# Kernel tuning notes

Measured on AMD Instinct MI355X. Metric: run time of the kernel, lower is better.

## Reference

```python
import jax, jax.numpy as jnp
import numpy as np

B = 64        # graphs per batch
N0 = 131072   # total nodes (2048 per graph)
E = 1048576   # total edges (within-graph)
H = 128       # hidden_size
C = 7         # class_num (input feature dim)
EPS = 1e-5


def setup_inputs() -> dict:
    key = jax.random.key(0)
    ks = jax.random.split(key, 16)
    n0 = N0 // B
    x = jax.random.normal(ks[0], (N0, C), dtype=jnp.float32)
    # within-graph random edges: edge e belongs to graph e // (E//B)
    g = jnp.repeat(jnp.arange(B, dtype=jnp.int32), E // B)
    row = jax.random.randint(ks[1], (E,), 0, n0, dtype=jnp.int32) + g * n0
    col = jax.random.randint(ks[2], (E,), 0, n0, dtype=jnp.int32) + g * n0
    edge_index = jnp.stack([row, col], axis=0)
    batch = jnp.repeat(jnp.arange(B, dtype=jnp.int32), n0)
    s = 0.05
    params = dict(
        Wc1=jax.random.normal(ks[3], (C, H), jnp.float32) * s,     # conv1 weight
        Wc=jax.random.normal(ks[4], (3, H, H), jnp.float32) * s,   # conv2-4 weights
        bc=jax.random.normal(ks[5], (4, H), jnp.float32) * s,      # conv biases
        Wf=jax.random.normal(ks[6], (4, H, H), jnp.float32) * s,   # fc weights
        bf=jax.random.normal(ks[7], (4, H), jnp.float32) * s,      # fc biases
        bn_g=jnp.ones((4, H), jnp.float32),                        # BN gamma
        bn_b=jnp.zeros((4, H), jnp.float32),                       # BN beta
        Ws1=jax.random.normal(ks[8], (4, H, 1), jnp.float32) * s,  # SAG GraphConv root weight
        Ws2=jax.random.normal(ks[9], (4, H, 1), jnp.float32) * s,  # SAG GraphConv neighbor weight
        bs=jax.random.normal(ks[10], (4, 1), jnp.float32) * s,     # SAG GraphConv bias
    )
    return dict(x=x, edge_index=edge_index, batch=batch, **params)


def _gcn_conv(x, W, b, row, col, m, N):
    # PyG GCNConv with self loops: out_i = sum_{j->i} h_j / sqrt(d_i d_j) + h_i / d_i + b
    h = x @ W
    deg = jax.ops.segment_sum(m, col, num_segments=N) + 1.0  # +1 for self loop
    dis = jax.lax.rsqrt(deg)
    norm = dis[row] * dis[col] * m  # masked-out edges contribute 0
    agg = jax.ops.segment_sum(h[row] * norm[:, None], col, num_segments=N)
    return agg + h * (dis * dis)[:, None] + b


def _sag_score(x, W1, W2, b, row, col, m, N):
    # GraphConv(H, 1, aggr='add'): score_i = W1^T x_i + W2^T sum_{j->i} x_j + b
    nbr = jax.ops.segment_sum(x[row] * m[:, None], col, num_segments=N)
    return (x @ W1 + nbr @ W2 + b).reshape(-1)


def _bn(x, g, b):
    mu = jnp.mean(x, axis=0)
    var = jnp.mean((x - mu) ** 2, axis=0)  # biased, matches torch BN training
    return (x - mu) * jax.lax.rsqrt(var + EPS) * g + b


def reference(x, edge_index, batch, Wc1, Wc, bc, Wf, bf, bn_g, bn_b, Ws1, Ws2, bs):
    row, col = edge_index[0], edge_index[1]
    m = jnp.ones(row.shape, x.dtype)  # edge validity mask (static-size edge list)
    n = x.shape[0] // B               # nodes per graph (equal-size graphs)
    for i in range(4):
        N = B * n
        W = Wc1 if i == 0 else Wc[i - 1]
        h = _gcn_conv(x, W, bc[i], row, col, m, N)
        h = jax.nn.relu(h @ Wf[i] + bf[i])
        h = _bn(h, bn_g[i], bn_b[i])
        # SAGPooling(ratio=0.5): per-graph top-k by GraphConv score, x *= tanh(score)
        score = _sag_score(h, Ws1[i], Ws2[i], bs[i], row, col, m, N)
        k = n // 2
        _, idx = jax.lax.top_k(score.reshape(B, n), k)  # [B, k] per-graph indices
        perm = (idx + jnp.arange(B, dtype=idx.dtype)[:, None] * n).reshape(-1)
        x = h[perm] * jnp.tanh(score[perm])[:, None]
        # re-index edges; mask edges touching removed nodes
        inv = jnp.full((N,), -1, dtype=row.dtype).at[perm].set(
            jnp.arange(B * k, dtype=row.dtype))
        nr, nc = inv[row], inv[col]
        valid = (nr >= 0) & (nc >= 0)
        m = m * valid.astype(m.dtype)
        row = jnp.where(valid, nr, 0)
        col = jnp.where(valid, nc, 0)
        n = k
    # global_mean_pool over block-structured batch -> [B, H]
    return x.reshape(B, n, -1).mean(axis=1)
```

## Files before the change

kernel.cpp:

```cpp
#include <hip/hip_runtime.h>
#include <cstdint>

#define HB 128
#define NB 64
#define NE 1048576
#define EG (NE / 256)

__global__ __launch_bounds__(256) void init_edges_k(const int* __restrict__ ei,
    int* __restrict__ row, int* __restrict__ col, int E) {
  int e = blockIdx.x * blockDim.x + threadIdx.x;
  if (e < E) { row[e] = ei[e]; col[e] = ei[E + e]; }
}

__global__ __launch_bounds__(128) void init_goff_k(int* __restrict__ goff, int epg) {
  int g = threadIdx.x;
  if (g <= NB) goff[g] = g * epg;
}

__global__ __launch_bounds__(256) void matmulK_k(const float* __restrict__ X,
    const float* __restrict__ W, const float* __restrict__ bias,
    float* __restrict__ out, int N, int K, int KS, int flags) {
  extern __shared__ float lw[];
  int tid = threadIdx.x;
  int nv = K * 32;
  for (int idx = tid; idx < nv; idx += 256)
    ((float4*)lw)[idx] = ((const float4*)W)[idx];
  __syncthreads();
  int tx = tid & 31, ty = tid >> 5;
  long rowbase = (long)blockIdx.x * 32;
  float acc[4][4] = {};
  const float* xp = X + (size_t)(rowbase + ty) * KS;
  for (int k = 0; k < K; ++k) {
    float4 wv = ((float4*)lw)[k * 32 + tx];
    #pragma unroll
    for (int rr = 0; rr < 4; ++rr) {
      float xv = xp[(size_t)rr * 8 * KS + k];
      acc[rr][0] += xv * wv.x; acc[rr][1] += xv * wv.y;
      acc[rr][2] += xv * wv.z; acc[rr][3] += xv * wv.w;
    }
  }
  float4 bv = make_float4(0.f, 0.f, 0.f, 0.f);
  if (flags & 1) bv = ((const float4*)bias)[tx];
  #pragma unroll
  for (int rr = 0; rr < 4; ++rr) {
    long r = rowbase + ty + rr * 8;
    float4 v;
    v.x = acc[rr][0] + bv.x; v.y = acc[rr][1] + bv.y;
    v.z = acc[rr][2] + bv.z; v.w = acc[rr][3] + bv.w;
    if (flags & 2) {
      v.x = fmaxf(v.x, 0.f); v.y = fmaxf(v.y, 0.f);
      v.z = fmaxf(v.z, 0.f); v.w = fmaxf(v.w, 0.f);
    }
    ((float4*)(out + (size_t)r * HB))[tx] = v;
  }
}

__global__ __launch_bounds__(256) void gemm128_k(const float* __restrict__ X,
    const float* __restrict__ W, const float* __restrict__ bias,
    float* __restrict__ out, int N, int flags,
    const int* __restrict__ sel, const float* __restrict__ scale,
    const float* __restrict__ bnsc, float* __restrict__ stat) {
  __shared__ float Xs[2][64][8];
  __shared__ float2 red[8][128];
  int tid = threadIdx.x;
  int tx = tid & 31;
  int ty = tid >> 5;
  long rowbase = (long)blockIdx.x * 64;
  float4 acc[8];
  #pragma unroll
  for (int r = 0; r < 8; ++r) acc[r] = make_float4(0.f, 0.f, 0.f, 0.f);
  int lr = tid >> 1, lq = (tid & 1) * 4;
  const float* xrow = nullptr;
  float lsc = 1.f;
  bool gmode = (flags & 4) != 0;
  if (tid < 128) {
    long srcrow = rowbase + lr;
    if (gmode) { srcrow = sel[rowbase + lr]; lsc = scale[rowbase + lr]; }
    xrow = X + (size_t)srcrow * HB + lq;
  }
  auto loadx = [&](int kc) -> float4 {
    float4 v = *(const float4*)(xrow + kc * 8);
    if (gmode) {
      int ch = kc * 8 + lq;
      float4 a = *(const float4*)(bnsc + ch);
      float4 b = *(const float4*)(bnsc + 128 + ch);
      v.x = (v.x * a.x + b.x) * lsc; v.y = (v.y * a.y + b.y) * lsc;
      v.z = (v.z * a.z + b.z) * lsc; v.w = (v.w * a.w + b.w) * lsc;
    } else {
      v.x *= lsc; v.y *= lsc; v.z *= lsc; v.w *= lsc;
    }
    return v;
  };
  if (tid < 128) *(float4*)&Xs[0][lr][lq] = loadx(0);
  __syncthreads();
  for (int kc = 0; kc < 16; ++kc) {
    int cur = kc & 1;
    if (kc < 15 && tid < 128)
      *(float4*)&Xs[cur ^ 1][lr][lq] = loadx(kc + 1);
    float4 wreg[8];
    #pragma unroll
    for (int k = 0; k < 8; ++k)
      wreg[k] = *(const float4*)(W + (size_t)(kc * 8 + k) * HB + 4 * tx);
    #pragma unroll
    for (int kk = 0; kk < 8; kk += 4) {
      float4 xreg[8];
      #pragma unroll
      for (int r = 0; r < 8; ++r)
        xreg[r] = *(const float4*)&Xs[cur][ty + 8 * r][kk];
      #pragma unroll
      for (int k = 0; k < 4; ++k) {
        #pragma unroll
        for (int r = 0; r < 8; ++r) {
          float xv = ((const float*)&xreg[r])[k];
          float4 wv = wreg[kk + k];
          acc[r].x += xv * wv.x; acc[r].y += xv * wv.y;
          acc[r].z += xv * wv.z; acc[r].w += xv * wv.w;
        }
      }
    }
    __syncthreads();
  }
  float4 bv = make_float4(0.f, 0.f, 0.f, 0.f);
  if (flags & 1) bv = ((const float4*)bias)[tx];
  float4 psum = make_float4(0.f, 0.f, 0.f, 0.f);
  float4 psq  = make_float4(0.f, 0.f, 0.f, 0.f);
  #pragma unroll
  for (int r = 0; r < 8; ++r) {
    float4 v;
    v.x = acc[r].x + bv.x; v.y = acc[r].y + bv.y;
    v.z = acc[r].z + bv.z; v.w = acc[r].w + bv.w;
    if (flags & 2) {
      v.x = fmaxf(v.x, 0.f); v.y = fmaxf(v.y, 0.f);
      v.z = fmaxf(v.z, 0.f); v.w = fmaxf(v.w, 0.f);
    }
    if (flags & 8) {
      psum.x += v.x; psum.y += v.y; psum.z += v.z; psum.w += v.w;
      psq.x += v.x * v.x; psq.y += v.y * v.y;
      psq.z += v.z * v.z; psq.w += v.w * v.w;
    }
    *(float4*)(out + (size_t)(rowbase + ty + 8 * r) * HB + 4 * tx) = v;
  }
  if (flags & 8) {
    red[ty][4 * tx + 0] = make_float2(psum.x, psq.x);
    red[ty][4 * tx + 1] = make_float2(psum.y, psq.y);
    red[ty][4 * tx + 2] = make_float2(psum.z, psq.z);
    red[ty][4 * tx + 3] = make_float2(psum.w, psq.w);
    __syncthreads();
    if (tid < 128) {
      float s = 0.f, q = 0.f;
      #pragma unroll
      for (int t = 0; t < 8; ++t) { s += red[t][tid].x; q += red[t][tid].y; }
      atomicAdd(&stat[tid], s);
      atomicAdd(&stat[128 + tid], q);
    }
  }
}

__global__ __launch_bounds__(1024) void csr_build_k(const int* __restrict__ row,
    const int* __restrict__ col, const int* __restrict__ goff,
    float* __restrict__ dis, int* __restrict__ off, int* __restrict__ srow,
    float* __restrict__ snorm, int n) {
  extern __shared__ int lds[];
  int* ldeg = lds;
  int* lsa  = lds + n;
  int* lsb  = lds + 2 * n;
  float* ldis = (float*)(lds + 3 * n);
  int g = blockIdx.x, tid = threadIdx.x;
  int e0 = goff[g], e1 = goff[g + 1];
  int base = g * n;
  for (int i = tid; i < n; i += 1024) ldeg[i] = 0;
  __syncthreads();
  for (int e = e0 + tid; e < e1; e += 1024) atomicAdd(&ldeg[col[e] - base], 1);
  __syncthreads();
  for (int i = tid; i < n; i += 1024) {
    int d = ldeg[i];
    ldis[i] = rsqrtf((float)d + 1.f);
    lsa[i] = d;
  }
  __syncthreads();
  int* src = lsa; int* dst = lsb;
  for (int o = 1; o < n; o <<= 1) {
    for (int i = tid; i < n; i += 1024) dst[i] = src[i] + ((i >= o) ? src[i - o] : 0);
    __syncthreads();
    int* t = src; src = dst; dst = t;
  }
  for (int i = tid; i < n; i += 1024) {
    int d = ldeg[i];
    int ex = src[i] - d;
    off[base + i] = e0 + ex;
    ldeg[i] = ex;
    dis[base + i] = ldis[i];
  }
  if (tid == 0) off[base + n] = e1;
  __syncthreads();
  for (int e = e0 + tid; e < e1; e += 1024) {
    int r = row[e], c = col[e];
    int lc = c - base;
    int p = e0 + atomicAdd(&ldeg[lc], 1);
    srow[p] = r;
    snorm[p] = ldis[r - base] * ldis[lc];
  }
}

__global__ __launch_bounds__(256) void agg7_k(const float* __restrict__ x,
    const int* __restrict__ srow, const float* __restrict__ snorm,
    const int* __restrict__ off, const float* __restrict__ dis,
    float* __restrict__ aggx, int N) {
  int gid = blockIdx.x * blockDim.x + threadIdx.x;
  int node = gid >> 3, c = gid & 7;
  if (node >= N) return;
  float acc = 0.f;
  if (c < 7) {
    int s = off[node], e = off[node + 1];
    for (int j = s; j < e; ++j) acc += x[(size_t)srow[j] * 7 + c] * snorm[j];
    float d = dis[node];
    acc += x[(size_t)node * 7 + c] * d * d;
  }
  aggx[(size_t)node * 8 + c] = acc;
}

__global__ __launch_bounds__(256) void gather_combine_k(const float* __restrict__ hw,
    const int* __restrict__ srow, const float* __restrict__ snorm,
    const int* __restrict__ off, const float* __restrict__ dis,
    const float* __restrict__ bc, float* __restrict__ out, int N) {
  int gid = blockIdx.x * blockDim.x + threadIdx.x;
  int node = gid >> 5;
  if (node >= N) return;
  int ch = (gid & 31) * 4;
  int s = off[node], e = off[node + 1];
  float4 acc = make_float4(0.f, 0.f, 0.f, 0.f);
  for (int j = s; j < e; ++j) {
    int r = srow[j];
    float nm = snorm[j];
    float4 v = *(const float4*)(hw + (size_t)r * HB + ch);
    acc.x += v.x * nm; acc.y += v.y * nm; acc.z += v.z * nm; acc.w += v.w * nm;
  }
  float d = dis[node], d2 = d * d;
  float4 h = *(const float4*)(hw + (size_t)node * HB + ch);
  float4 b = *(const float4*)(bc + ch);
  acc.x += h.x * d2 + b.x; acc.y += h.y * d2 + b.y;
  acc.z += h.z * d2 + b.z; acc.w += h.w * d2 + b.w;
  *(float4*)(out + (size_t)node * HB + ch) = acc;
}

__global__ __launch_bounds__(128) void bnfin_k(float* __restrict__ stat,
    const float* __restrict__ g, const float* __restrict__ b,
    float* __restrict__ sc, int N) {
  int c = threadIdx.x;
  if (c < 128) {
    float mu = stat[c] / N, ms = stat[128 + c] / N;
    float var = ms - mu * mu;
    float a = g[c] * rsqrtf(var + 1e-5f);
    sc[c] = a;
    sc[128 + c] = b[c] - mu * a;
    stat[c] = 0.f;
    stat[128 + c] = 0.f;
  }
}

__global__ __launch_bounds__(256) void score_prep_k(const float* __restrict__ h,
    const float* __restrict__ sc, const float* __restrict__ w1,
    const float* __restrict__ w2, float* __restrict__ selfs,
    float* __restrict__ t2, int N) {
  int gid = blockIdx.x * blockDim.x + threadIdx.x;
  int node = gid >> 6;
  if (node >= N) return;
  int lane = gid & 63, c = lane * 2;
  float2 v = *(const float2*)(h + (size_t)node * HB + c);
  v.x = v.x * sc[c] + sc[128 + c];
  v.y = v.y * sc[c + 1] + sc[128 + c + 1];
  float s1 = v.x * w1[c] + v.y * w1[c + 1];
  float s2 = v.x * w2[c] + v.y * w2[c + 1];
  #pragma unroll
  for (int off = 32; off > 0; off >>= 1) {
    s1 += __shfl_xor(s1, off);
    s2 += __shfl_xor(s2, off);
  }
  if (lane == 0) { selfs[node] = s1; t2[node] = s2; }
}

__global__ __launch_bounds__(256) void score_k(const float* __restrict__ selfs,
    const float* __restrict__ t2, const int* __restrict__ srow,
    const int* __restrict__ off, const float* __restrict__ bs,
    float* __restrict__ score, int N) {
  int i = blockIdx.x * blockDim.x + threadIdx.x;
  if (i >= N) return;
  float s = selfs[i] + bs[0];
  int e0 = off[i], e1 = off[i + 1];
  for (int j = e0; j < e1; ++j) s += t2[srow[j]];
  score[i] = s;
}

__global__ __launch_bounds__(256) void rank_topk_k(const float* __restrict__ score,
    int* __restrict__ inv, int* __restrict__ sel, float* __restrict__ scale,
    int n, int k, int bpg) {
  extern __shared__ float ls[];
  int g = blockIdx.x / bpg, sub = blockIdx.x % bpg;
  int tid = threadIdx.x;
  const float* sg = score + (size_t)g * n;
  for (int i = tid; i < n; i += 256) ls[i] = sg[i];
  __syncthreads();
  int i0 = sub * 256 + tid;
  float s0 = ls[i0];
  int r0 = 0;
  for (int jb = 0; jb < n; jb += 4) {
    float4 v = *(const float4*)(ls + jb);
    r0 += (v.x > s0) || (v.x == s0 && (jb + 0) < i0);
    r0 += (v.y > s0) || (v.y == s0 && (jb + 1) < i0);
    r0 += (v.z > s0) || (v.z == s0 && (jb + 2) < i0);
    r0 += (v.w > s0) || (v.w == s0 && (jb + 3) < i0);
  }
  if (r0 < k) {
    inv[(size_t)g * n + i0] = g * k + r0;
    sel[(size_t)g * k + r0] = g * n + i0;
    scale[(size_t)g * k + r0] = tanhf(s0);
  } else inv[(size_t)g * n + i0] = -1;
}

__global__ __launch_bounds__(256) void gather_x_k(const float* __restrict__ h,
    const float* __restrict__ bnsc, const int* __restrict__ sel,
    const float* __restrict__ scale, float* __restrict__ xout, int M) {
  int gid = blockIdx.x * blockDim.x + threadIdx.x;
  int r = gid >> 5;
  if (r >= M) return;
  int ch = (gid & 31) * 4;
  int old = sel[r];
  float sc = scale[r];
  float4 v = *(const float4*)(h + (size_t)old * HB + ch);
  float4 a = *(const float4*)(bnsc + ch);
  float4 b = *(const float4*)(bnsc + 128 + ch);
  v.x = (v.x * a.x + b.x) * sc; v.y = (v.y * a.y + b.y) * sc;
  v.z = (v.z * a.z + b.z) * sc; v.w = (v.w * a.w + b.w) * sc;
  *(float4*)(xout + (size_t)r * HB + ch) = v;
}

__global__ __launch_bounds__(256) void cmpA_k(const int* __restrict__ row,
    const int* __restrict__ col, const int* __restrict__ inv,
    const int* __restrict__ ecnt, int* __restrict__ bcnt) {
  int e = blockIdx.x * 256 + threadIdx.x;
  bool valid = false;
  if (e < *ecnt) {
    int nr = inv[row[e]], nc = inv[col[e]];
    valid = (nr >= 0) && (nc >= 0);
  }
  unsigned long long mask = __ballot(valid);
  __shared__ int ws[4];
  int lane = threadIdx.x & 63, wid = threadIdx.x >> 6;
  if (lane == 0) ws[wid] = __popcll(mask);
  __syncthreads();
  if (threadIdx.x == 0) bcnt[blockIdx.x] = ws[0] + ws[1] + ws[2] + ws[3];
}

__global__ __launch_bounds__(1024) void cmpB_k(const int* __restrict__ bcnt,
    int* __restrict__ bbase, int* __restrict__ total) {
  __shared__ int s[1024];
  int tid = threadIdx.x;
  int v0 = bcnt[4 * tid], v1 = bcnt[4 * tid + 1];
  int v2 = bcnt[4 * tid + 2], v3 = bcnt[4 * tid + 3];
  int tsum = v0 + v1 + v2 + v3;
  s[tid] = tsum; __syncthreads();
  for (int o = 1; o < 1024; o <<= 1) {
    int t = (tid >= o) ? s[tid - o] : 0;
    __syncthreads();
    s[tid] += t;
    __syncthreads();
  }
  int base = s[tid] - tsum;
  bbase[4 * tid] = base;
  bbase[4 * tid + 1] = base + v0;
  bbase[4 * tid + 2] = base + v0 + v1;
  bbase[4 * tid + 3] = base + v0 + v1 + v2;
  if (tid == 1023) *total = s[1023];
}

__global__ __launch_bounds__(256) void cmpC_k(const int* __restrict__ row,
    const int* __restrict__ col, const int* __restrict__ inv,
    const int* __restrict__ ecnt, const int* __restrict__ bbase,
    int* __restrict__ nrow, int* __restrict__ ncol, int* __restrict__ gcnt,
    int khalf) {
  int e = blockIdx.x * 256 + threadIdx.x;
  bool valid = false; int nr = 0, nc = 0;
  if (e < *ecnt) {
    nr = inv[row[e]]; nc = inv[col[e]];
    valid = (nr >= 0) && (nc >= 0);
  }
  unsigned long long mask = __ballot(valid);
  int lane = threadIdx.x & 63, wid = threadIdx.x >> 6;
  __shared__ int ws[4];
  __shared__ int lg[NB];
  if (threadIdx.x < NB) lg[threadIdx.x] = 0;
  if (lane == 0) ws[wid] = __popcll(mask);
  __syncthreads();
  if (threadIdx.x == 0) {
    int a = ws[0], b = ws[1], c2 = ws[2];
    ws[0] = 0; ws[1] = a; ws[2] = a + b; ws[3] = a + b + c2;
  }
  __syncthreads();
  if (valid) {
    unsigned long long lt = ((unsigned long long)1 << lane) - 1;
    int pos = bbase[blockIdx.x] + ws[wid] + (int)__popcll(mask & lt);
    nrow[pos] = nr;
    ncol[pos] = nc;
    atomicAdd(&lg[nc / khalf], 1);
  }
  __syncthreads();
  if (threadIdx.x < NB && lg[threadIdx.x]) atomicAdd(&gcnt[threadIdx.x], lg[threadIdx.x]);
}

__global__ void gscan_k(int* __restrict__ gcnt, int* __restrict__ goff) {
  if (threadIdx.x == 0) {
    int s = 0;
    for (int g = 0; g < NB; ++g) { goff[g] = s; s += gcnt[g]; gcnt[g] = 0; }
    goff[NB] = s;
  }
}

__global__ __launch_bounds__(128) void pool_k(const float* __restrict__ x,
    float* __restrict__ out, int n) {
  int g = blockIdx.x, c = threadIdx.x;
  float s = 0.f;
  for (int r = 0; r < n; ++r) s += x[((size_t)g * n + r) * HB + c];
  out[g * HB + c] = s / n;
}

extern "C" void kernel_launch(void* const* d_in, const int* in_sizes, int n_in,
                              void* d_out, int out_size, void* d_ws, size_t ws_size,
                              hipStream_t stream) {
  const float* x_in = (const float*)d_in[0];
  const int*   ei   = (const int*)d_in[1];
  const float* Wc1  = (const float*)d_in[3];
  const float* Wc   = (const float*)d_in[4];
  const float* bc   = (const float*)d_in[5];
  const float* Wf   = (const float*)d_in[6];
  const float* bf   = (const float*)d_in[7];
  const float* bng  = (const float*)d_in[8];
  const float* bnb  = (const float*)d_in[9];
  const float* Ws1  = (const float*)d_in[10];
  const float* Ws2  = (const float*)d_in[11];
  const float* bs   = (const float*)d_in[12];

  const int N0 = 131072, E = NE;
  char* p = (char*)d_ws;
  auto alloc = [&](size_t bytes) -> char* {
    char* r = p; p += (bytes + 255) & ~(size_t)255; return r;
  };
  float* A    = (float*)alloc((size_t)N0 * HB * 4);
  float* Bb   = (float*)alloc((size_t)N0 * HB * 4);
  float* Cc   = (float*)alloc((size_t)(N0 / 2) * HB * 4);
  float* aggx = (float*)alloc((size_t)N0 * 8 * 4);
  int*   rowA = (int*)alloc((size_t)E * 4);
  int*   colA = (int*)alloc((size_t)E * 4);
  int*   rowB = (int*)alloc((size_t)E * 4);
  int*   colB = (int*)alloc((size_t)E * 4);
  float* dis  = (float*)alloc((size_t)N0 * 4);
  float* selfs= (float*)alloc((size_t)N0 * 4);
  float* t2v  = (float*)alloc((size_t)N0 * 4);
  float* score= (float*)alloc((size_t)N0 * 4);
  int*   inv  = (int*)alloc((size_t)N0 * 4);
  int*   off  = (int*)alloc((size_t)(N0 + 1) * 4);
  int*   sel  = (int*)alloc((size_t)(N0 / 2) * 4);
  float* scale= (float*)alloc((size_t)(N0 / 2) * 4);
  int*   bcnt = (int*)alloc((size_t)EG * 4);
  int*   bbase= (int*)alloc((size_t)EG * 4);
  int*   gcnt = (int*)alloc(NB * 4);
  int*   goffA= (int*)alloc((NB + 1) * 4);
  int*   goffB= (int*)alloc((NB + 1) * 4);
  float* stat = (float*)alloc(256 * 4);
  float* bnsc = (float*)alloc(256 * 4);

  hipMemsetAsync(stat, 0, 256 * 4, stream);
  hipMemsetAsync(gcnt, 0, NB * 4, stream);

  init_edges_k<<<E / 256, 256, 0, stream>>>(ei, rowA, colA, E);
  init_goff_k<<<1, 128, 0, stream>>>(goffA, E / NB);

  int* rowCur = rowA; int* colCur = colA;
  int* rowNxt = rowB; int* colNxt = colB;
  int* goffCur = goffA; int* goffNxt = goffB;

  int n = 2048;
  for (int i = 0; i < 4; ++i) {
    int N = NB * n, khalf = n >> 1;
    int*   srow  = rowNxt;
    float* snorm = (float*)colNxt;
    csr_build_k<<<NB, 1024, (size_t)16 * n, stream>>>(
        rowCur, colCur, goffCur, dis, off, srow, snorm, n);
    if (i == 0) {
      agg7_k<<<N / 32, 256, 0, stream>>>(x_in, srow, snorm, off, dis, aggx, N);
      matmulK_k<<<N / 32, 256, (size_t)7 * HB * 4, stream>>>(
          aggx, Wc1, bc, Bb, N, 7, 8, 1);
    } else {
      const float* W = Wc + (size_t)(i - 1) * HB * HB;
      gemm128_k<<<N / 64, 256, 0, stream>>>(A, W, nullptr, Cc, N, 4,
                                            sel, scale, bnsc, nullptr);
      gather_combine_k<<<N / 8, 256, 0, stream>>>(Cc, srow, snorm, off, dis,
                                                  bc + (size_t)i * HB, Bb, N);
    }
    gemm128_k<<<N / 64, 256, 0, stream>>>(
        Bb, Wf + (size_t)i * HB * HB, bf + (size_t)i * HB, A, N, 1 | 2 | 8,
        nullptr, nullptr, nullptr, stat);
    bnfin_k<<<1, 128, 0, stream>>>(stat, bng + (size_t)i * HB, bnb + (size_t)i * HB, bnsc, N);
    score_prep_k<<<N / 4, 256, 0, stream>>>(
        A, bnsc, Ws1 + (size_t)i * HB, Ws2 + (size_t)i * HB, selfs, t2v, N);
    score_k<<<(N + 255) / 256, 256, 0, stream>>>(selfs, t2v, srow, off, bs + i, score, N);
    int bpg = n / 256;
    rank_topk_k<<<NB * bpg, 256, (size_t)n * 4, stream>>>(
        score, inv, sel, scale, n, khalf, bpg);
    if (i < 3) {
      cmpA_k<<<EG, 256, 0, stream>>>(rowCur, colCur, inv, goffCur + NB, bcnt);
      cmpB_k<<<1, 1024, 0, stream>>>(bcnt, bbase, goffNxt + NB);
      cmpC_k<<<EG, 256, 0, stream>>>(rowCur, colCur, inv, goffCur + NB, bbase,
                                     rowNxt, colNxt, gcnt, khalf);
      gscan_k<<<1, 64, 0, stream>>>(gcnt, goffNxt);
      int* t;
      t = rowCur; rowCur = rowNxt; rowNxt = t;
      t = colCur; colCur = colNxt; colNxt = t;
      t = goffCur; goffCur = goffNxt; goffNxt = t;
    } else {
      gather_x_k<<<(NB * khalf) / 8, 256, 0, stream>>>(
          A, bnsc, sel, scale, Cc, NB * khalf);
    }
    n = khalf;
  }
  pool_k<<<NB, 128, 0, stream>>>(Cc, (float*)d_out, n);
}
```

Baseline: 693.8 us.

## Fuse layer-0 conv and fc GEMMs, shard BN stats, drop small scan kernels

Layer 0's 7-wide conv matmul and the following 128x128 fc GEMM with ReLU and BN-stat accumulation are merged into one kernel. The intermediate tile stays in LDS instead of going through a global buffer. BN statistics are spread over 8 atomic shards per layer, with pre-zeroed per-layer buffers, so bnfin no longer has to clear them. The gscan and init_goff kernels are removed: csr_build now computes each graph's edge offset with a serial per-block prefix over per-layer counts. This saves launches and global traffic at the cost of a small serial loop in thread 0 of each CSR block.

```diff
diff --git a/kernel.cpp b/kernel.cpp
--- a/kernel.cpp
+++ b/kernel.cpp
@@ -7,51 +7,104 @@
 #define EG (NE / 256)
 
 __global__ __launch_bounds__(256) void init_edges_k(const int* __restrict__ ei,
-    int* __restrict__ row, int* __restrict__ col, int E) {
+    int* __restrict__ row, int* __restrict__ col, int* __restrict__ gcnt0,
+    int* __restrict__ ecnt0, int E) {
   int e = blockIdx.x * blockDim.x + threadIdx.x;
   if (e < E) { row[e] = ei[e]; col[e] = ei[E + e]; }
-}
-
-__global__ __launch_bounds__(128) void init_goff_k(int* __restrict__ goff, int epg) {
-  int g = threadIdx.x;
-  if (g <= NB) goff[g] = g * epg;
-}
-
-__global__ __launch_bounds__(256) void matmulK_k(const float* __restrict__ X,
-    const float* __restrict__ W, const float* __restrict__ bias,
-    float* __restrict__ out, int N, int K, int KS, int flags) {
-  extern __shared__ float lw[];
+  if (blockIdx.x == 0) {
+    if (threadIdx.x < NB) gcnt0[threadIdx.x] = E / NB;
+    if (threadIdx.x == 0) *ecnt0 = E;
+  }
+}
+
+__global__ __launch_bounds__(256) void conv_fc0_k(const float* __restrict__ aggx,
+    const float* __restrict__ Wc1, const float* __restrict__ bc0,
+    const float* __restrict__ Wf, const float* __restrict__ bf0,
+    float* __restrict__ out, int N, float* __restrict__ stat) {
+  __shared__ float lt[64][128];
+  __shared__ float laggx[64][8];
+  __shared__ float lwc1[7 * 128];
+  float2 (*red)[128] = (float2(*)[128])lt;
   int tid = threadIdx.x;
-  int nv = K * 32;
-  for (int idx = tid; idx < nv; idx += 256)
-    ((float4*)lw)[idx] = ((const float4*)W)[idx];
-  __syncthreads();
   int tx = tid & 31, ty = tid >> 5;
-  long rowbase = (long)blockIdx.x * 32;
-  float acc[4][4] = {};
-  const float* xp = X + (size_t)(rowbase + ty) * KS;
-  for (int k = 0; k < K; ++k) {
-    float4 wv = ((float4*)lw)[k * 32 + tx];
-    #pragma unroll
-    for (int rr = 0; rr < 4; ++rr) {
-      float xv = xp[(size_t)rr * 8 * KS + k];
-      acc[rr][0] += xv * wv.x; acc[rr][1] += xv * wv.y;
-      acc[rr][2] += xv * wv.z; acc[rr][3] += xv * wv.w;
-    }
-  }
-  float4 bv = make_float4(0.f, 0.f, 0.f, 0.f);
-  if (flags & 1) bv = ((const float4*)bias)[tx];
-  #pragma unroll
-  for (int rr = 0; rr < 4; ++rr) {
-    long r = rowbase + ty + rr * 8;
+  long rowbase = (long)blockIdx.x * 64;
+  for (int i = tid; i < 7 * 32; i += 256)
+    ((float4*)lwc1)[i] = ((const float4*)Wc1)[i];
+  if (tid < 128) {
+    int lr = tid >> 1, lq = (tid & 1) * 4;
+    *(float4*)&laggx[lr][lq] = *(const float4*)(aggx + (rowbase + lr) * 8 + lq);
+  }
+  __syncthreads();
+  float4 tacc[8];
+  float4 bcv = ((const float4*)bc0)[tx];
+  #pragma unroll
+  for (int r = 0; r < 8; ++r) tacc[r] = bcv;
+  #pragma unroll
+  for (int k = 0; k < 7; ++k) {
+    float4 wv = ((float4*)lwc1)[k * 32 + tx];
+    #pragma unroll
+    for (int r = 0; r < 8; ++r) {
+      float xv = laggx[ty + 8 * r][k];
+      tacc[r].x += xv * wv.x; tacc[r].y += xv * wv.y;
+      tacc[r].z += xv * wv.z; tacc[r].w += xv * wv.w;
+    }
+  }
+  #pragma unroll
+  for (int r = 0; r < 8; ++r)
+    *(float4*)&lt[ty + 8 * r][4 * tx] = tacc[r];
+  __syncthreads();
+  float4 acc[8];
+  #pragma unroll
+  for (int r = 0; r < 8; ++r) acc[r] = make_float4(0.f, 0.f, 0.f, 0.f);
+  for (int kc = 0; kc < 16; ++kc) {
+    float4 wreg[8];
+    #pragma unroll
+    for (int k = 0; k < 8; ++k)
+      wreg[k] = *(const float4*)(Wf + (size_t)(kc * 8 + k) * HB + 4 * tx);
+    #pragma unroll
+    for (int kk = 0; kk < 8; kk += 4) {
+      float4 xreg[8];
+      #pragma unroll
+      for (int r = 0; r < 8; ++r)
+        xreg[r] = *(const float4*)&lt[ty + 8 * r][kc * 8 + kk];
+      #pragma unroll
+      for (int k2 = 0; k2 < 4; ++k2) {
+        #pragma unroll
+        for (int r = 0; r < 8; ++r) {
+          float xv = ((const float*)&xreg[r])[k2];
+          float4 wv = wreg[kk + k2];
+          acc[r].x += xv * wv.x; acc[r].y += xv * wv.y;
+          acc[r].z += xv * wv.z; acc[r].w += xv * wv.w;
+        }
+      }
+    }
+  }
+  float4 bv = ((const float4*)bf0)[tx];
+  float4 psum = make_float4(0.f, 0.f, 0.f, 0.f);
+  float4 psq  = make_float4(0.f, 0.f, 0.f, 0.f);
+  __syncthreads();
+  #pragma unroll
+  for (int r = 0; r < 8; ++r) {
     float4 v;
-    v.x = acc[rr][0] + bv.x; v.y = acc[rr][1] + bv.y;
-    v.z = acc[rr][2] + bv.z; v.w = acc[rr][3] + bv.w;
-    if (flags & 2) {
-      v.x = fmaxf(v.x, 0.f); v.y = fmaxf(v.y, 0.f);
-      v.z = fmaxf(v.z, 0.f); v.w = fmaxf(v.w, 0.f);
-    }
-    ((float4*)(out + (size_t)r * HB))[tx] = v;
+    v.x = fmaxf(acc[r].x + bv.x, 0.f); v.y = fmaxf(acc[r].y + bv.y, 0.f);
+    v.z = fmaxf(acc[r].z + bv.z, 0.f); v.w = fmaxf(acc[r].w + bv.w, 0.f);
+    psum.x += v.x; psum.y += v.y; psum.z += v.z; psum.w += v.w;
+    psq.x += v.x * v.x; psq.y += v.y * v.y;
+    psq.z += v.z * v.z; psq.w += v.w * v.w;
+    *(float4*)(out + (size_t)(rowbase + ty + 8 * r) * HB + 4 * tx) = v;
+  }
+  red[ty][4 * tx + 0] = make_float2(psum.x, psq.x);
+  red[ty][4 * tx + 1] = make_float2(psum.y, psq.y);
+  red[ty][4 * tx + 2] = make_float2(psum.z, psq.z);
+  red[ty][4 * tx + 3] = make_float2(psum.w, psq.w);
+  __syncthreads();
+  if (tid < 128) {
+    float s = 0.f, q = 0.f;
+    #pragma unroll
+    for (int t = 0; t < 8; ++t) { s += red[t][tid].x; q += red[t][tid].y; }
+    float* st = stat + ((blockIdx.x & 7) << 8);
+    atomicAdd(&st[tid], s);
+    atomicAdd(&st[128 + tid], q);
   }
 }
 
@@ -60,8 +113,8 @@
     float* __restrict__ out, int N, int flags,
     const int* __restrict__ sel, const float* __restrict__ scale,
     const float* __restrict__ bnsc, float* __restrict__ stat) {
-  __shared__ float Xs[2][64][8];
   __shared__ float2 red[8][128];
+  float (*Xs)[64][8] = (float(*)[64][8])red;
   int tid = threadIdx.x;
   int tx = tid & 31;
   int ty = tid >> 5;
@@ -86,8 +139,6 @@
       float4 b = *(const float4*)(bnsc + 128 + ch);
       v.x = (v.x * a.x + b.x) * lsc; v.y = (v.y * a.y + b.y) * lsc;
       v.z = (v.z * a.z + b.z) * lsc; v.w = (v.w * a.w + b.w) * lsc;
-    } else {
-      v.x *= lsc; v.y *= lsc; v.z *= lsc; v.w *= lsc;
     }
     return v;
   };
@@ -150,14 +201,15 @@
       float s = 0.f, q = 0.f;
       #pragma unroll
       for (int t = 0; t < 8; ++t) { s += red[t][tid].x; q += red[t][tid].y; }
-      atomicAdd(&stat[tid], s);
-      atomicAdd(&stat[128 + tid], q);
+      float* st = stat + ((blockIdx.x & 7) << 8);
+      atomicAdd(&st[tid], s);
+      atomicAdd(&st[128 + tid], q);
     }
   }
 }
 
 __global__ __launch_bounds__(1024) void csr_build_k(const int* __restrict__ row,
-    const int* __restrict__ col, const int* __restrict__ goff,
+    const int* __restrict__ col, const int* __restrict__ gcnt,
     float* __restrict__ dis, int* __restrict__ off, int* __restrict__ srow,
     float* __restrict__ snorm, int n) {
   extern __shared__ int lds[];
@@ -165,11 +217,17 @@
   int* lsa  = lds + n;
   int* lsb  = lds + 2 * n;
   float* ldis = (float*)(lds + 3 * n);
+  __shared__ int e01[2];
   int g = blockIdx.x, tid = threadIdx.x;
-  int e0 = goff[g], e1 = goff[g + 1];
+  if (tid == 0) {
+    int s = 0;
+    for (int gg = 0; gg < g; ++gg) s += gcnt[gg];
+    e01[0] = s; e01[1] = s + gcnt[g];
+  }
   int base = g * n;
   for (int i = tid; i < n; i += 1024) ldeg[i] = 0;
   __syncthreads();
+  int e0 = e01[0], e1 = e01[1];
   for (int e = e0 + tid; e < e1; e += 1024) atomicAdd(&ldeg[col[e] - base], 1);
   __syncthreads();
   for (int i = tid; i < n; i += 1024) {
@@ -243,18 +301,22 @@
   *(float4*)(out + (size_t)node * HB + ch) = acc;
 }
 
-__global__ __launch_bounds__(128) void bnfin_k(float* __restrict__ stat,
+__global__ __launch_bounds__(128) void bnfin_k(const float* __restrict__ stat8,
     const float* __restrict__ g, const float* __restrict__ b,
     float* __restrict__ sc, int N) {
   int c = threadIdx.x;
   if (c < 128) {
-    float mu = stat[c] / N, ms = stat[128 + c] / N;
-    float var = ms - mu * mu;
+    float s = 0.f, q = 0.f;
+    #pragma unroll
+    for (int sh = 0; sh < 8; ++sh) {
+      s += stat8[sh * 256 + c];
+      q += stat8[sh * 256 + 128 + c];
+    }
+    float mu = s / N;
+    float var = q / N - mu * mu;
     float a = g[c] * rsqrtf(var + 1e-5f);
     sc[c] = a;
     sc[128 + c] = b[c] - mu * a;
-    stat[c] = 0.f;
-    stat[128 + c] = 0.f;
   }
 }
 
@@ -405,14 +467,6 @@
   }
   __syncthreads();
   if (threadIdx.x < NB && lg[threadIdx.x]) atomicAdd(&gcnt[threadIdx.x], lg[threadIdx.x]);
-}
-
-__global__ void gscan_k(int* __restrict__ gcnt, int* __restrict__ goff) {
-  if (threadIdx.x == 0) {
-    int s = 0;
-    for (int g = 0; g < NB; ++g) { goff[g] = s; s += gcnt[g]; gcnt[g] = 0; }
-    goff[NB] = s;
-  }
 }
 
 __global__ __launch_bounds__(128) void pool_k(const float* __restrict__ x,
@@ -462,44 +516,42 @@
   float* scale= (float*)alloc((size_t)(N0 / 2) * 4);
   int*   bcnt = (int*)alloc((size_t)EG * 4);
   int*   bbase= (int*)alloc((size_t)EG * 4);
-  int*   gcnt = (int*)alloc(NB * 4);
-  int*   goffA= (int*)alloc((NB + 1) * 4);
-  int*   goffB= (int*)alloc((NB + 1) * 4);
-  float* stat = (float*)alloc(256 * 4);
+  int*   gcntL= (int*)alloc(4 * NB * 4);
+  float* stat8= (float*)alloc(4 * 8 * 256 * 4);
   float* bnsc = (float*)alloc(256 * 4);
-
-  hipMemsetAsync(stat, 0, 256 * 4, stream);
-  hipMemsetAsync(gcnt, 0, NB * 4, stream);
-
-  init_edges_k<<<E / 256, 256, 0, stream>>>(ei, rowA, colA, E);
-  init_goff_k<<<1, 128, 0, stream>>>(goffA, E / NB);
+  int*   ecnt = (int*)alloc(2 * 4);
+
+  hipMemsetAsync(stat8, 0, 4 * 8 * 256 * 4, stream);
+  hipMemsetAsync(gcntL, 0, 4 * NB * 4, stream);
+
+  init_edges_k<<<E / 256, 256, 0, stream>>>(ei, rowA, colA, gcntL, ecnt, E);
 
   int* rowCur = rowA; int* colCur = colA;
   int* rowNxt = rowB; int* colNxt = colB;
-  int* goffCur = goffA; int* goffNxt = goffB;
+  int* ecntCur = ecnt; int* ecntNxt = ecnt + 1;
 
   int n = 2048;
   for (int i = 0; i < 4; ++i) {
     int N = NB * n, khalf = n >> 1;
+    float* statL = stat8 + (size_t)i * 8 * 256;
     int*   srow  = rowNxt;
     float* snorm = (float*)colNxt;
     csr_build_k<<<NB, 1024, (size_t)16 * n, stream>>>(
-        rowCur, colCur, goffCur, dis, off, srow, snorm, n);
+        rowCur, colCur, gcntL + i * NB, dis, off, srow, snorm, n);
     if (i == 0) {
       agg7_k<<<N / 32, 256, 0, stream>>>(x_in, srow, snorm, off, dis, aggx, N);
-      matmulK_k<<<N / 32, 256, (size_t)7 * HB * 4, stream>>>(
-          aggx, Wc1, bc, Bb, N, 7, 8, 1);
+      conv_fc0_k<<<N / 64, 256, 0, stream>>>(aggx, Wc1, bc, Wf, bf, A, N, statL);
     } else {
       const float* W = Wc + (size_t)(i - 1) * HB * HB;
       gemm128_k<<<N / 64, 256, 0, stream>>>(A, W, nullptr, Cc, N, 4,
                                             sel, scale, bnsc, nullptr);
       gather_combine_k<<<N / 8, 256, 0, stream>>>(Cc, srow, snorm, off, dis,
                                                   bc + (size_t)i * HB, Bb, N);
-    }
-    gemm128_k<<<N / 64, 256, 0, stream>>>(
-        Bb, Wf + (size_t)i * HB * HB, bf + (size_t)i * HB, A, N, 1 | 2 | 8,
-        nullptr, nullptr, nullptr, stat);
-    bnfin_k<<<1, 128, 0, stream>>>(stat, bng + (size_t)i * HB, bnb + (size_t)i * HB, bnsc, N);
+      gemm128_k<<<N / 64, 256, 0, stream>>>(
+          Bb, Wf + (size_t)i * HB * HB, bf + (size_t)i * HB, A, N, 1 | 2 | 8,
+          nullptr, nullptr, nullptr, statL);
+    }
+    bnfin_k<<<1, 128, 0, stream>>>(statL, bng + (size_t)i * HB, bnb + (size_t)i * HB, bnsc, N);
     score_prep_k<<<N / 4, 256, 0, stream>>>(
         A, bnsc, Ws1 + (size_t)i * HB, Ws2 + (size_t)i * HB, selfs, t2v, N);
     score_k<<<(N + 255) / 256, 256, 0, stream>>>(selfs, t2v, srow, off, bs + i, score, N);
@@ -507,15 +559,14 @@
     rank_topk_k<<<NB * bpg, 256, (size_t)n * 4, stream>>>(
         score, inv, sel, scale, n, khalf, bpg);
     if (i < 3) {
-      cmpA_k<<<EG, 256, 0, stream>>>(rowCur, colCur, inv, goffCur + NB, bcnt);
-      cmpB_k<<<1, 1024, 0, stream>>>(bcnt, bbase, goffNxt + NB);
-      cmpC_k<<<EG, 256, 0, stream>>>(rowCur, colCur, inv, goffCur + NB, bbase,
-                                     rowNxt, colNxt, gcnt, khalf);
-      gscan_k<<<1, 64, 0, stream>>>(gcnt, goffNxt);
+      cmpA_k<<<EG, 256, 0, stream>>>(rowCur, colCur, inv, ecntCur, bcnt);
+      cmpB_k<<<1, 1024, 0, stream>>>(bcnt, bbase, ecntNxt);
+      cmpC_k<<<EG, 256, 0, stream>>>(rowCur, colCur, inv, ecntCur, bbase,
+                                     rowNxt, colNxt, gcntL + (i + 1) * NB, khalf);
       int* t;
       t = rowCur; rowCur = rowNxt; rowNxt = t;
       t = colCur; colCur = colNxt; colNxt = t;
-      t = goffCur; goffCur = goffNxt; goffNxt = t;
+      t = ecntCur; ecntCur = ecntNxt; ecntNxt = t;
     } else {
       gather_x_k<<<(NB * khalf) / 8, 256, 0, stream>>>(
           A, bnsc, sel, scale, Cc, NB * khalf);
```

Result: faster. 635.8 us (-8.4%).
